# Kernel optimization log

Hardware: AMD Instinct MI355X
Metric: run time of the kernel (lower is better)

The kernel has to match this reference:

```python
import jax, jax.numpy as jnp
import numpy as np

N_HEADS = 16


def _rope(q, k, freq_cos, freq_sin):
    # q,k: [B,S,H,hd]; freqs: [S, hd//2]
    B, S, H, hd = q.shape
    qr, qi = q.reshape(B, S, H, hd // 2, 2)[..., 0], q.reshape(B, S, H, hd // 2, 2)[..., 1]
    kr, ki = k.reshape(B, S, H, hd // 2, 2)[..., 0], k.reshape(B, S, H, hd // 2, 2)[..., 1]
    fc = freq_cos[None, :, None, :]  # [1,S,1,hd//2]
    fs = freq_sin[None, :, None, :]
    q_out = jnp.stack([qr * fc - qi * fs, qr * fs + qi * fc], axis=-1).reshape(B, S, H, hd)
    k_out = jnp.stack([kr * fc - ki * fs, kr * fs + ki * fc], axis=-1).reshape(B, S, H, hd)
    return q_out, k_out


def setup_inputs() -> dict:
    key = jax.random.key(0)
    ks = jax.random.split(key, 7)
    B, S, D = 2, 2048, 2048
    hd = D // N_HEADS
    scale = 1.0 / np.sqrt(D)
    return {
        "x": jax.random.normal(ks[0], (B, S, D), dtype=jnp.float32),
        "freq_cos": jnp.cos(jax.random.normal(ks[1], (S, hd // 2), dtype=jnp.float32)),
        "freq_sin": jnp.sin(jax.random.normal(ks[2], (S, hd // 2), dtype=jnp.float32)),
        "wq": jax.random.normal(ks[3], (D, D), dtype=jnp.float32) * scale,
        "wk": jax.random.normal(ks[4], (D, D), dtype=jnp.float32) * scale,
        "wv": jax.random.normal(ks[5], (D, D), dtype=jnp.float32) * scale,
        "wo": jax.random.normal(ks[6], (D, D), dtype=jnp.float32) * scale,
    }


def reference(x, freq_cos, freq_sin, wq, wk, wv, wo):
    B, S, D = x.shape
    H = N_HEADS
    hd = D // H
    # torch nn.Linear(weight [out,in]): y = x @ W^T
    q = (x @ wq.T).reshape(B, S, H, hd)
    k = (x @ wk.T).reshape(B, S, H, hd)
    v = (x @ wv.T).reshape(B, S, H, hd)
    q, k = _rope(q, k, freq_cos, freq_sin)
    # [B,H,S,hd]
    q = q.transpose(0, 2, 1, 3)
    k = k.transpose(0, 2, 1, 3)
    v = v.transpose(0, 2, 1, 3)
    scores = jnp.einsum("bhqd,bhkd->bhqk", q, k) / jnp.sqrt(jnp.float32(hd))
    causal = jnp.triu(jnp.full((S, S), -jnp.inf, dtype=scores.dtype), k=1)
    scores = scores + causal[None, None, :, :]
    probs = jax.nn.softmax(scores, axis=-1)
    out = jnp.einsum("bhqk,bhkd->bhqd", probs, v)
    out = out.transpose(0, 2, 1, 3).reshape(B, S, D)
    return out @ wo.T
```

## Files before the change

kernel.cpp:

```cpp
#include <hip/hip_runtime.h>
#include <hip/hip_bf16.h>
#include <stdint.h>

typedef unsigned short u16;
typedef unsigned int   u32;

typedef __attribute__((ext_vector_type(8))) short bf16x8;
typedef __attribute__((ext_vector_type(4))) float f32x4;
typedef __attribute__((ext_vector_type(4))) float f4;
typedef __attribute__((ext_vector_type(4))) u16   u16x4;

#define GLOBAL_AS __attribute__((address_space(1)))
#define LDS_AS    __attribute__((address_space(3)))

#define QSCALE (0.088388347648318447f * 1.4426950408889634f)

__device__ __forceinline__ void gload_lds16(const void* gsrc, void* ldst) {
    __builtin_amdgcn_global_load_lds((GLOBAL_AS const u32*)gsrc,
                                     (LDS_AS u32*)ldst, 16, 0, 0);
}

__device__ __forceinline__ float b2f(u16 u) {
    union { u32 i; float f; } x; x.i = ((u32)u) << 16; return x.f;
}
__device__ __forceinline__ u16 f2b(float f) {
    u32 u = __builtin_bit_cast(u32, f);
    u = (u + 0x7fff + ((u >> 16) & 1)) >> 16;
    return (u16)u;
}
__device__ __forceinline__ u16 f2b_tr(float f) {
    return (u16)(__builtin_bit_cast(u32, f) >> 16);
}

__global__ __launch_bounds__(256)
void f2bf_all(const float* __restrict__ x,  const float* __restrict__ wq,
              const float* __restrict__ wk, const float* __restrict__ wv,
              const float* __restrict__ wo, u16* __restrict__ out,
              int md4, int dd4, int n4) {
    int i = blockIdx.x * blockDim.x + threadIdx.x;
    if (i >= n4) return;
    const float* src; int off;
    if (i < md4) { src = x; off = i; }
    else {
        int j = i - md4;
        int k = j / dd4;
        off = j - k * dd4;
        src = (k == 0) ? wq : (k == 1) ? wk : (k == 2) ? wv : wo;
    }
    f4 v = ((const f4*)src)[off];
    u16x4 o;
    o[0] = f2b(v[0]); o[1] = f2b(v[1]); o[2] = f2b(v[2]); o[3] = f2b(v[3]);
    ((u16x4*)out)[i] = o;
}

#define BARR() do { asm volatile("" ::: "memory"); \
                    __builtin_amdgcn_s_barrier();  \
                    asm volatile("" ::: "memory"); } while (0)

template<int OUT_MODE>
__global__ __launch_bounds__(512, 2)
void gemm8(const u16* __restrict__ A, const u16* __restrict__ B,
           void* __restrict__ Cptr, int M, int N, int Kdim,
           const float* __restrict__ fc, const float* __restrict__ fs) {
    __shared__ char lds[131072];
    const int t = threadIdx.x, l = t & 63, w = t >> 6;
    const int g = l >> 4, r16 = l & 15;
    const int wm = w >> 2, wn = w & 3;

    const int nwg = gridDim.x * gridDim.y;
    const int id  = blockIdx.y * gridDim.x + blockIdx.x;
    const int swz = (id & 7) * (nwg >> 3) + (id >> 3);
    const int bx  = swz % gridDim.x, by = swz / gridDim.x;
    const int m0 = by * 256, n0 = bx * 256;

    f32x4 acc[8][4];
#pragma unroll
    for (int i = 0; i < 8; i++)
#pragma unroll
        for (int j = 0; j < 4; j++) acc[i][j] = (f32x4){0.f, 0.f, 0.f, 0.f};

    const int sw  = (r16 & 7) << 4;
    const int cK0 = (g * 16) ^ sw;
    const int cK1 = (64 + g * 16) ^ sw;

    bf16x8 afA[4][2], bfA[2][2], bfB[2][2];

    auto stgA = [&](int d, int r, int kt) {
#pragma unroll
        for (int i = 0; i < 2; i++) {
            const int o  = (i * 8 + w) * 1024 + l * 16;
            const int rr = o >> 7;
            const int cb = (o & 127) ^ ((rr & 7) << 4);
            const int gr = ((rr >> 6) << 7) + r * 64 + (rr & 63);
            gload_lds16(A + (size_t)(m0 + gr) * Kdim + kt * 64 + (cb >> 1),
                        lds + d * 65536 + r * 16384 + (i * 8 + w) * 1024);
        }
    };
    auto stgB = [&](int d, int r, int kt) {
#pragma unroll
        for (int i = 0; i < 2; i++) {
            const int o  = (i * 8 + w) * 1024 + l * 16;
            const int rr = o >> 7;
            const int cb = (o & 127) ^ ((rr & 7) << 4);
            const int gc = ((rr >> 5) << 6) + r * 32 + (rr & 31);
            gload_lds16(B + (size_t)(n0 + gc) * Kdim + kt * 64 + (cb >> 1),
                        lds + d * 65536 + 32768 + r * 16384 + (i * 8 + w) * 1024);
        }
    };
    auto rdA = [&](int d, int qm) {
#pragma unroll
        for (int mi = 0; mi < 4; mi++) {
            const char* p = lds + d * 65536 + qm * 16384
                            + (wm * 64 + mi * 16 + r16) * 128;
            afA[mi][0] = *(const bf16x8*)(p + cK0);
            afA[mi][1] = *(const bf16x8*)(p + cK1);
        }
    };
    auto rdB = [&](bf16x8 (&dst)[2][2], int d, int qn) {
#pragma unroll
        for (int ni = 0; ni < 2; ni++) {
            const char* p = lds + d * 65536 + 32768 + qn * 16384
                            + (wn * 32 + ni * 16 + r16) * 128;
            dst[ni][0] = *(const bf16x8*)(p + cK0);
            dst[ni][1] = *(const bf16x8*)(p + cK1);
        }
    };
    auto mm = [&](int qm, int qn, bf16x8 (&bf)[2][2]) {
        __builtin_amdgcn_s_setprio(1);
#pragma unroll
        for (int kk = 0; kk < 2; kk++)
#pragma unroll
            for (int mi = 0; mi < 4; mi++)
#pragma unroll
                for (int ni = 0; ni < 2; ni++)
                    acc[qm * 4 + mi][qn * 2 + ni] =
                        __builtin_amdgcn_mfma_f32_16x16x32_bf16(
                            afA[mi][kk], bf[ni][kk],
                            acc[qm * 4 + mi][qn * 2 + ni], 0, 0, 0);
        __builtin_amdgcn_s_setprio(0);
    };

    const int nk = Kdim >> 6;

    stgA(0, 0, 0); stgB(0, 1, 0); stgB(0, 0, 0); stgA(0, 1, 0);
    stgA(1, 0, 1); stgB(1, 1, 1);
    asm volatile("s_waitcnt vmcnt(4)" ::: "memory");
    BARR();

    for (int tt = 0; tt < (nk >> 1); ++tt) {
        const int b1 = (2 * tt + 1);
        const int a2 = (2 * tt + 2) & (nk - 1);
        const int b2 = (2 * tt + 3) & (nk - 1);

        rdA(0, 0); rdB(bfA, 0, 0); stgB(1, 0, b1); BARR();
        mm(0, 0, bfA);
        rdB(bfB, 0, 1); stgA(1, 1, b1); BARR();
        mm(0, 1, bfB);
        rdA(0, 1); stgA(0, 0, a2); BARR();
        mm(1, 1, bfB);
        stgB(0, 1, a2);
        asm volatile("s_waitcnt vmcnt(4)" ::: "memory");
        BARR();
        mm(1, 0, bfA);
        rdA(1, 0); rdB(bfA, 1, 0); stgB(0, 0, a2); BARR();
        mm(0, 0, bfA);
        rdB(bfB, 1, 1); stgA(0, 1, a2); BARR();
        mm(0, 1, bfB);
        rdA(1, 1); stgA(1, 0, b2); BARR();
        mm(1, 1, bfB);
        stgB(1, 1, b2);
        asm volatile("s_waitcnt vmcnt(4)" ::: "memory");
        BARR();
        mm(1, 0, bfA);
    }

    if (OUT_MODE == 2 && n0 < 4096) {
        asm volatile("s_waitcnt vmcnt(0)" ::: "memory");
        __builtin_amdgcn_s_barrier();
        const char* fcb = (const char*)(fc + (size_t)(m0 & 2047) * 64);
        const char* fsb = (const char*)(fs + (size_t)(m0 & 2047) * 64);
#pragma unroll
        for (int q = 0; q < 8; q++) {
            gload_lds16(fcb + q * 8192 + w * 1024 + l * 16,
                        lds + q * 8192 + w * 1024);
            gload_lds16(fsb + q * 8192 + w * 1024 + l * 16,
                        lds + 65536 + q * 8192 + w * 1024);
        }
        asm volatile("s_waitcnt vmcnt(0)" ::: "memory");
        __builtin_amdgcn_s_barrier();
    }

#pragma unroll
    for (int a = 0; a < 8; a++)
#pragma unroll
        for (int b = 0; b < 4; b++)
#pragma unroll
            for (int r = 0; r < 4; r++) {
                int row = m0 + wm * 128 + a * 16 + g * 4 + r;
                int col = n0 + wn * 64 + b * 16 + r16;
                float v = acc[a][b][r];
                if (OUT_MODE == 0) {
                    ((float*)Cptr)[(size_t)row * N + col] = v;
                } else {
                    float ov = v;
                    if (n0 < 4096) {
                        float part = __shfl_xor(v, 1);
                        const int ss = wm * 128 + a * 16 + g * 4 + r;
                        const int i  = ((wn * 64 + b * 16 + r16) & 127) >> 1;
                        const int fo = (ss * 64 + i) << 2;
                        float c  = *(const float*)(lds + fo);
                        float sn = *(const float*)(lds + 65536 + fo);
                        ov = (r16 & 1) ? (part * sn + v * c) : (v * c - part * sn);
                        if (n0 < 2048) ov *= QSCALE;
                    }
                    ((u16*)Cptr)[(size_t)row * N + col] = f2b(ov);
                }
            }
}

template<int OUT_MODE>
__global__ __launch_bounds__(512, 2)
void gemm_bt(const u16* __restrict__ A, const u16* __restrict__ B,
             void* __restrict__ Cptr, int M, int N, int Kdim) {
    __shared__ char lds[3][49152];
    const int t = threadIdx.x, l = t & 63, w = t >> 6;
    const int g = l >> 4, r16 = l & 15;

    const int nwg = gridDim.x * gridDim.y;
    const int id  = blockIdx.y * gridDim.x + blockIdx.x;
    const int swz = (id & 7) * (nwg >> 3) + (id >> 3);
    const int bx  = swz % gridDim.x, by = swz / gridDim.x;
    const int m0 = by * 256, n0 = bx * 128;
    const int wm = w >> 1, wn = w & 1;
    const int rA = wm * 64, rB = wn * 64;

    f32x4 acc[4][4];
#pragma unroll
    for (int i = 0; i < 4; i++)
#pragma unroll
        for (int j = 0; j < 4; j++) acc[i][j] = (f32x4){0.f, 0.f, 0.f, 0.f};

    const int nk = Kdim >> 6;

    auto stage = [&](int kt, int bi) {
        const int k0 = kt << 6;
#pragma unroll
        for (int q = 0; q < 4; q++) {
            const int o = q * 8192 + w * 1024 + l * 16;
            const int row = o >> 7;
            const int cb = (o & 127) ^ ((row & 7) << 4);
            gload_lds16(A + (size_t)(m0 + row) * Kdim + k0 + (cb >> 1),
                        &lds[bi][q * 8192 + w * 1024]);
        }
#pragma unroll
        for (int q = 0; q < 2; q++) {
            const int o = q * 8192 + w * 1024 + l * 16;
            const int row = o >> 7;
            const int cb = (o & 127) ^ ((row & 7) << 4);
            gload_lds16(B + (size_t)(n0 + row) * Kdim + k0 + (cb >> 1),
                        &lds[bi][32768 + q * 8192 + w * 1024]);
        }
    };

    stage(0, 0);
    stage(1, 1);

    for (int kt = 0; kt < nk; ++kt) {
        const int cur = kt % 3;
        __builtin_amdgcn_sched_barrier(0);
        __builtin_amdgcn_s_barrier();
        stage((kt + 2) % nk, (kt + 2) % 3);
        asm volatile("s_waitcnt vmcnt(12)" ::: "memory");
        __builtin_amdgcn_s_barrier();
        __builtin_amdgcn_sched_barrier(0);

        const char* Ab = lds[cur];
        const char* Bb = lds[cur] + 32768;
        bf16x8 af[2][4], bfr[2][4];
#pragma unroll
        for (int kk = 0; kk < 2; kk++)
#pragma unroll
            for (int i = 0; i < 4; i++) {
                const int rowa = rA + i * 16 + r16;
                const int cba = (kk * 64 + g * 16) ^ ((rowa & 7) << 4);
                af[kk][i] = *(const bf16x8*)(Ab + rowa * 128 + cba);
                const int rowb = rB + i * 16 + r16;
                const int cbb = (kk * 64 + g * 16) ^ ((rowb & 7) << 4);
                bfr[kk][i] = *(const bf16x8*)(Bb + rowb * 128 + cbb);
            }
#pragma unroll
        for (int kk = 0; kk < 2; kk++)
#pragma unroll
            for (int mi = 0; mi < 4; mi++)
#pragma unroll
                for (int ni = 0; ni < 4; ni++)
                    acc[mi][ni] = __builtin_amdgcn_mfma_f32_16x16x32_bf16(af[kk][mi],
                                                                          bfr[kk][ni],
                                                                          acc[mi][ni], 0, 0, 0);
    }

#pragma unroll
    for (int mi = 0; mi < 4; mi++)
#pragma unroll
        for (int ni = 0; ni < 4; ni++)
#pragma unroll
            for (int r = 0; r < 4; r++) {
                int row = m0 + rA + mi * 16 + g * 4 + r;
                int col = n0 + rB + ni * 16 + r16;
                float v = acc[mi][ni][r];
                if (OUT_MODE == 0)      ((float*)Cptr)[(size_t)row * N + col] = v;
                else                    ((u16*)Cptr)[(size_t)row * N + col] = f2b(v);
            }
}

__global__ __launch_bounds__(512, 2)
void flash_attn(const u16* __restrict__ QKV, u16* __restrict__ Op) {
    const int S = 2048, DQ = 6144, DO = 2048;
    __shared__ u16 kbuf[16384];
    __shared__ u16 vtlds[128 * 136];
    const int t = threadIdx.x, l = t & 63, w = t >> 6;
    const int g = l >> 4, r16 = l & 15;
    const int bh = blockIdx.x, b = bh >> 4, h = bh & 15;
    const int tq = 15 - (int)blockIdx.y;
    const int q0 = tq * 128;
    const int nkt = tq + 1;
    const size_t base = ((size_t)(b * S)) * DQ + h * 128;
    const u16* qp = QKV + base;
    const u16* kp = qp + 2048;
    const u16* vp = qp + 4096;
    const size_t obase = ((size_t)(b * S)) * DO + h * 128;

    bf16x8 qf[4];
#pragma unroll
    for (int ks = 0; ks < 4; ks++)
        qf[ks] = *(const bf16x8*)(qp + (size_t)(q0 + w * 16 + r16) * DQ
                                  + ks * 32 + g * 8);

    f32x4 acc[8];
#pragma unroll
    for (int i = 0; i < 8; i++) acc[i] = (f32x4){0.f, 0.f, 0.f, 0.f};
    float m_run[4], s_run[4];
#pragma unroll
    for (int r = 0; r < 4; r++) { m_run[r] = -3.0e38f; s_run[r] = 0.f; }

    auto stageK = [&](int kv0) {
#pragma unroll
        for (int i = 0; i < 4; i++) {
            const int o = (w * 4 + i) * 1024 + l * 16;
            const int row = o >> 8;
            const int cb = (o & 255) ^ ((row & 7) << 4);
            gload_lds16(kp + (size_t)(kv0 + row) * DQ + (cb >> 1),
                        (char*)kbuf + (w * 4 + i) * 1024);
        }
    };
    bf16x8 vv[2][2];
    auto loadV = [&](int kv0) {
#pragma unroll
        for (int c = 0; c < 2; c++)
#pragma unroll
            for (int kh = 0; kh < 2; kh++)
                vv[c][kh] = *(const bf16x8*)(vp + (size_t)(kv0 + kh * 64 + l) * DQ
                                             + (w * 16 + c * 8));
    };
    auto writeVT = [&]() {
#pragma unroll
        for (int c = 0; c < 2; c++)
#pragma unroll
            for (int kh = 0; kh < 2; kh++) {
                const int d0 = w * 16 + c * 8;
#pragma unroll
                for (int j = 0; j < 8; j++)
                    vtlds[(d0 + j) * 136 + kh * 64 + l] = (u16)vv[c][kh][j];
            }
    };

    stageK(0);
    loadV(0);
    asm volatile("s_waitcnt vmcnt(0)" ::: "memory");
    __syncthreads();
    writeVT();
    __syncthreads();

    for (int kt = 0; kt < nkt; ++kt) {
        const int kv0 = kt * 128;
        const bool more = (kt + 1 < nkt);
        if (more) loadV(kv0 + 128);

        f32x4 sf[8];
#pragma unroll
        for (int nf = 0; nf < 8; nf++) sf[nf] = (f32x4){0.f, 0.f, 0.f, 0.f};
#pragma unroll
        for (int nf = 0; nf < 8; nf++) {
            const int row = nf * 16 + r16;
            const int rb = row * 256;
#pragma unroll
            for (int ks = 0; ks < 4; ks++) {
                const int cb = (ks * 64 + g * 16) ^ ((row & 7) << 4);
                bf16x8 kf = *(const bf16x8*)((const char*)kbuf + rb + cb);
                sf[nf] = __builtin_amdgcn_mfma_f32_16x16x32_bf16(qf[ks], kf,
                                                                 sf[nf], 0, 0, 0);
            }
        }

        const bool diag = (kt == tq);
        float mt[4];
#pragma unroll
        for (int r = 0; r < 4; r++) mt[r] = -3.0e38f;
#pragma unroll
        for (int nf = 0; nf < 8; nf++)
#pragma unroll
            for (int r = 0; r < 4; r++) {
                float s = sf[nf][r];
                if (diag) {
                    int qrow = q0 + w * 16 + g * 4 + r;
                    int kcol = kv0 + nf * 16 + r16;
                    if (kcol > qrow) s = -3.0e38f;
                }
                sf[nf][r] = s;
                mt[r] = fmaxf(mt[r], s);
            }
#pragma unroll
        for (int r = 0; r < 4; r++) {
#pragma unroll
            for (int d = 1; d < 16; d <<= 1)
                mt[r] = fmaxf(mt[r], __shfl_xor(mt[r], d));
        }
        int grow = (mt[0] > m_run[0] + 8.f) | (mt[1] > m_run[1] + 8.f) |
                   (mt[2] > m_run[2] + 8.f) | (mt[3] > m_run[3] + 8.f);
        if (__any(grow)) {
#pragma unroll
            for (int r = 0; r < 4; r++) {
                float mn = fmaxf(m_run[r], mt[r]);
                float alpha = exp2f(m_run[r] - mn);
                m_run[r] = mn;
                s_run[r] *= alpha;
#pragma unroll
                for (int i = 0; i < 8; i++) acc[i][r] *= alpha;
            }
        }

        __syncthreads();

        float psum[4];
#pragma unroll
        for (int r = 0; r < 4; r++) psum[r] = 0.f;
#pragma unroll
        for (int nf = 0; nf < 8; nf++)
#pragma unroll
            for (int r = 0; r < 4; r++) {
                float p = exp2f(sf[nf][r] - m_run[r]);
                psum[r] += p;
                const int prow = g * 4 + r;
                kbuf[w * 2048 + prow * 128 +
                     ((nf * 16 + r16) ^ ((prow & 7) << 3))] = f2b_tr(p);
            }
#pragma unroll
        for (int r = 0; r < 4; r++) {
#pragma unroll
            for (int d = 1; d < 16; d <<= 1)
                psum[r] += __shfl_xor(psum[r], d);
            s_run[r] += psum[r];
        }

        __builtin_amdgcn_s_setprio(1);
#pragma unroll
        for (int ks2 = 0; ks2 < 4; ks2++) {
            bf16x8 pf = *(const bf16x8*)(&kbuf[w * 2048 + r16 * 128 +
                                               ((ks2 * 32 + g * 8) ^ ((r16 & 7) << 3))]);
#pragma unroll
            for (int nf8 = 0; nf8 < 8; nf8++) {
                bf16x8 vf = *(const bf16x8*)(&vtlds[(nf8 * 16 + r16) * 136
                                                     + ks2 * 32 + g * 8]);
                acc[nf8] = __builtin_amdgcn_mfma_f32_16x16x32_bf16(pf, vf,
                                                                   acc[nf8], 0, 0, 0);
            }
        }
        __builtin_amdgcn_s_setprio(0);

        __syncthreads();
        if (more) {
            stageK(kv0 + 128);
            asm volatile("s_waitcnt vmcnt(8)" ::: "memory");
            writeVT();
            asm volatile("s_waitcnt vmcnt(0)" ::: "memory");
        }
        __syncthreads();
    }

    float inv[4];
#pragma unroll
    for (int r = 0; r < 4; r++) inv[r] = 1.0f / s_run[r];
#pragma unroll
    for (int nf8 = 0; nf8 < 8; nf8++)
#pragma unroll
        for (int r = 0; r < 4; r++) {
            size_t idx = obase + (size_t)(q0 + w * 16 + g * 4 + r) * DO
                         + nf8 * 16 + r16;
            Op[idx] = f2b(acc[nf8][r] * inv[r]);
        }
}

extern "C" void kernel_launch(void* const* d_in, const int* in_sizes, int n_in,
                              void* d_out, int out_size, void* d_ws, size_t ws_size,
                              hipStream_t stream) {
    const float* x  = (const float*)d_in[0];
    const float* fc = (const float*)d_in[1];
    const float* fs = (const float*)d_in[2];
    const float* wq = (const float*)d_in[3];
    const float* wk = (const float*)d_in[4];
    const float* wv = (const float*)d_in[5];
    const float* wo = (const float*)d_in[6];
    float* out = (float*)d_out;

    const int S = 2048, D = 2048;
    const int M = 2 * S;
    const size_t MD = (size_t)M * D;
    const size_t DD = (size_t)D * D;

    u16* xb   = (u16*)d_ws;
    u16* wqb  = xb  + MD;
    u16* wob  = wqb + 3 * DD;
    u16* qkvb = wob + DD;

    const int md4 = (int)(MD / 4), dd4 = (int)(DD / 4);
    const int n4  = md4 + 4 * dd4;
    f2bf_all<<<(n4 + 255) / 256, 256, 0, stream>>>(x, wq, wk, wv, wo, xb,
                                                   md4, dd4, n4);

    gemm8<2><<<dim3(6144 / 256, M / 256), 512, 0, stream>>>(xb, wqb, qkvb,
                                                            M, 6144, D, fc, fs);

    flash_attn<<<dim3(32, 16), 512, 0, stream>>>(qkvb, xb);

    gemm_bt<0><<<dim3(D / 128, M / 256), 512, 0, stream>>>(xb, wob, out, M, D, D);
}
```

Measured before the change: 276.0 us.

## Peel last GEMM k-iteration and overlap RoPE table loads with tail MMAs

```diff
diff --git a/kernel.cpp b/kernel.cpp
--- a/kernel.cpp
+++ b/kernel.cpp
@@ -141,16 +141,17 @@
     };
 
     const int nk = Kdim >> 6;
+    const bool rope = (OUT_MODE == 2) && (n0 < 4096);
 
     stgA(0, 0, 0); stgB(0, 1, 0); stgB(0, 0, 0); stgA(0, 1, 0);
     stgA(1, 0, 1); stgB(1, 1, 1);
     asm volatile("s_waitcnt vmcnt(4)" ::: "memory");
     BARR();
 
-    for (int tt = 0; tt < (nk >> 1); ++tt) {
+    for (int tt = 0; tt < (nk >> 1) - 1; ++tt) {
         const int b1 = (2 * tt + 1);
-        const int a2 = (2 * tt + 2) & (nk - 1);
-        const int b2 = (2 * tt + 3) & (nk - 1);
+        const int a2 = (2 * tt + 2);
+        const int b2 = (2 * tt + 3);
 
         rdA(0, 0); rdB(bfA, 0, 0); stgB(1, 0, b1); BARR();
         mm(0, 0, bfA);
@@ -174,18 +175,45 @@
         mm(1, 0, bfA);
     }
 
-    if (OUT_MODE == 2 && n0 < 4096) {
-        asm volatile("s_waitcnt vmcnt(0)" ::: "memory");
-        __builtin_amdgcn_s_barrier();
+    {
+        const int b1 = nk - 1;
         const char* fcb = (const char*)(fc + (size_t)(m0 & 2047) * 64);
         const char* fsb = (const char*)(fs + (size_t)(m0 & 2047) * 64);
-#pragma unroll
-        for (int q = 0; q < 8; q++) {
-            gload_lds16(fcb + q * 8192 + w * 1024 + l * 16,
-                        lds + q * 8192 + w * 1024);
-            gload_lds16(fsb + q * 8192 + w * 1024 + l * 16,
-                        lds + 65536 + q * 8192 + w * 1024);
-        }
+
+        rdA(0, 0); rdB(bfA, 0, 0); stgB(1, 0, b1); BARR();
+        mm(0, 0, bfA);
+        rdB(bfB, 0, 1); stgA(1, 1, b1); BARR();
+        mm(0, 1, bfB);
+        rdA(0, 1); BARR();
+        mm(1, 1, bfB);
+        if (rope) {
+#pragma unroll
+            for (int q = 0; q < 8; q++)
+                gload_lds16(fcb + q * 8192 + w * 1024 + l * 16,
+                            lds + q * 8192 + w * 1024);
+            asm volatile("s_waitcnt vmcnt(8)" ::: "memory");
+        } else {
+            asm volatile("s_waitcnt vmcnt(0)" ::: "memory");
+        }
+        BARR();
+        mm(1, 0, bfA);
+        rdA(1, 0); rdB(bfA, 1, 0); BARR();
+        mm(0, 0, bfA);
+        rdB(bfB, 1, 1); BARR();
+        mm(0, 1, bfB);
+        rdA(1, 1); BARR();
+        mm(1, 1, bfB);
+        if (rope) {
+#pragma unroll
+            for (int q = 0; q < 8; q++)
+                gload_lds16(fsb + q * 8192 + w * 1024 + l * 16,
+                            lds + 65536 + q * 8192 + w * 1024);
+        }
+        BARR();
+        mm(1, 0, bfA);
+    }
+
+    if (rope) {
         asm volatile("s_waitcnt vmcnt(0)" ::: "memory");
         __builtin_amdgcn_s_barrier();
     }
@@ -203,7 +231,7 @@
                     ((float*)Cptr)[(size_t)row * N + col] = v;
                 } else {
                     float ov = v;
-                    if (n0 < 4096) {
+                    if (rope) {
                         float part = __shfl_xor(v, 1);
                         const int ss = wm * 128 + a * 16 + g * 4 + r;
                         const int i  = ((wn * 64 + b * 16 + r16) & 127) >> 1;
```

Result: no change. 279.1 us (+1.2%).
